# Kernel tuning notes

Measured on AMD Instinct MI355X. Metric: run time of the kernel, lower is better.

Reference implementation:

```python
import jax, jax.numpy as jnp
import numpy as np

EPS = 1e-5

def l2norm(x, axis=-1):
    # matches torch F.normalize(p=2): denom clamped at 1e-12
    n = jnp.linalg.norm(x, axis=axis, keepdims=True)
    return x / jnp.maximum(n, 1e-12)

def setup_inputs() -> dict:
    key = jax.random.key(0)
    ks = jax.random.split(key, 10)
    B, N, D, P = 8, 1024, 128, 16
    context = jax.random.normal(ks[0], (B, N, D), jnp.float32)
    acc_u = jax.random.normal(ks[1], (B, N, 1), jnp.float32)
    acc_v = jax.random.normal(ks[2], (B, N, 1), jnp.float32)
    uv_angle = jax.random.normal(ks[3], (B, N, 1), jnp.float32)
    uv_angleACC = jax.random.normal(ks[4], (B, N, 1), jnp.float32)
    speed = jax.random.normal(ks[5], (B, N, 1), jnp.float32)
    dist = jax.random.uniform(ks[6], (N, N), jnp.float32)
    angle = jax.random.normal(ks[7], (N, N), jnp.float32)
    # xavier_uniform for weight_tensor [P, D]: bound = sqrt(6/(P+D))
    bound = float(np.sqrt(6.0 / (P + D)))
    weight_tensor = jax.random.uniform(ks[8], (P, D), jnp.float32, -bound, bound)
    return {"context": context, "acc_u": acc_u, "acc_v": acc_v,
            "uv_angle": uv_angle, "uv_angleACC": uv_angleACC, "speed": speed,
            "isPhy": 1, "dist": dist, "angle": angle,
            "weight_tensor": weight_tensor}

def reference(context, acc_u, acc_v, uv_angle, uv_angleACC, speed, isPhy, dist, angle, weight_tensor):
    gamma, theta, sigma = 1.4, 0.5, 0.5
    P = weight_tensor.shape[0]
    N = context.shape[1]
    # --- weighted-cosine multi-perspective attention ---
    w = weight_tensor[:, None, None, :]                 # [P,1,1,D]
    context_fc = context[None] * w                      # [P,B,N,D]
    context_norm = l2norm(context_fc)                   # [P,B,N,D]
    # matmul over perspectives then mean over P
    attention = jnp.einsum('pbnd,pbmd->bnm', context_norm, context_norm) / P
    # --- epsilon neighbourhood (epsilon=0, markoff=0), mask detached ---
    mask = jax.lax.stop_gradient((attention > 0.0).astype(attention.dtype))
    attention = attention * mask
    # --- wind dynamics (pred_var 'u', isPhy True, dist given) ---
    Acc = acc_u * acc_u + acc_v * acc_v                 # [B,N,1]
    x1 = jnp.sqrt(Acc[:, :, 0] + EPS)                   # [B,N]
    x2 = jnp.abs(jnp.cos(uv_angleACC[:, :, 0] - uv_angle[:, :, 0]))
    temp_acc = x1 * x2                                  # [B,N]
    acc_part = temp_acc[:, :, None] * jnp.eye(N, dtype=attention.dtype)  # diag [B,N,N]
    spd = jax.lax.stop_gradient(speed)                  # speed.detach()
    ang = jax.lax.stop_gradient(angle)[None]            # torch.tensor() detaches
    d = jax.lax.stop_gradient(dist)[None] + EPS
    # uv_angle/speed broadcast [B,N,1] -> [B,N,N] (repeat along last dim)
    selfwind = jnp.abs(spd) * jnp.abs(jnp.cos(ang - uv_angle) + sigma * acc_part) / d
    selfwind = l2norm(selfwind)                         # [B,N,N]
    y = gamma * jnp.einsum('bnk,bmk->bnm', selfwind, selfwind) / 20.0 + EPS
    y = l2norm(y)
    u = l2norm(jnp.abs(theta * selfwind + jnp.sqrt(y)) + EPS)
    return attention * u
```

## Files before the change

kernel.cpp:

```cpp
#include <hip/hip_runtime.h>
#include <hip/hip_bf16.h>
#include <math.h>

#define EPSV 1e-5f
#define AS1 __attribute__((address_space(1)))
#define AS3 __attribute__((address_space(3)))

typedef __attribute__((ext_vector_type(4))) float f32x4;
typedef __attribute__((ext_vector_type(8))) short bf16x8;
typedef __attribute__((ext_vector_type(4))) unsigned short u16x4;

__device__ __forceinline__ unsigned short f2b(float x) {
  union { float f; unsigned int u; } v; v.f = x;
  unsigned int r = v.u + 0x7FFFu + ((v.u >> 16) & 1u);
  return (unsigned short)(r >> 16);
}
__device__ __forceinline__ float b2f(unsigned short h) {
  union { float f; unsigned int u; } v; v.u = ((unsigned int)h) << 16;
  return v.f;
}

__device__ __forceinline__ float block_reduce_sum(float v, float* sbuf) {
  #pragma unroll
  for (int off = 32; off; off >>= 1) v += __shfl_xor(v, off);
  __syncthreads();
  if ((threadIdx.x & 63) == 0) sbuf[threadIdx.x >> 6] = v;
  __syncthreads();
  return sbuf[0] + sbuf[1] + sbuf[2] + sbuf[3];
}

__global__ __launch_bounds__(256) void prep(const float* __restrict__ ctx,
                                            const float* __restrict__ wt,
                                            const float* __restrict__ speed,
                                            const float* __restrict__ uva,
                                            const float* __restrict__ accu,
                                            const float* __restrict__ accv,
                                            const float* __restrict__ uvaACC,
                                            const float* __restrict__ angle,
                                            const float* __restrict__ dist,
                                            unsigned short* __restrict__ V,
                                            unsigned short* __restrict__ SW,
                                            int N) {
  __shared__ float sbuf[4];
  const int bn = blockIdx.x;
  const int tid = threadIdx.x;

  {
    const int w = tid >> 6;
    const int lane = tid & 63;
    const int p = w * 4 + (lane >> 4);
    const int dl = (lane & 15) * 8;
    const float* c = ctx + (size_t)bn * 128;
    const f32x4 ca = *(const f32x4*)(c + dl);
    const f32x4 cb = *(const f32x4*)(c + dl + 4);
    const f32x4 wa = *(const f32x4*)(wt + p * 128 + dl);
    const f32x4 wb = *(const f32x4*)(wt + p * 128 + dl + 4);
    float a[8];
    float ss = 0.0f;
    #pragma unroll
    for (int i = 0; i < 4; ++i) {
      a[i] = ca[i] * wa[i];
      a[4 + i] = cb[i] * wb[i];
      ss += a[i] * a[i] + a[4 + i] * a[4 + i];
    }
    ss += __shfl_xor(ss, 1);
    ss += __shfl_xor(ss, 2);
    ss += __shfl_xor(ss, 4);
    ss += __shfl_xor(ss, 8);
    const float inv = 1.0f / fmaxf(sqrtf(ss), 1e-12f);
    bf16x8 o;
    #pragma unroll
    for (int i = 0; i < 8; ++i) o[i] = (short)f2b(a[i] * inv);
    *(bf16x8*)(V + (size_t)bn * 2048 + p * 128 + dl) = o;
  }

  {
    const int n = bn & (N - 1);
    const float ua = uva[bn];
    const float sp = fabsf(speed[bn]);
    const float au = accu[bn], av = accv[bn];
    const float ta = sqrtf(au * au + av * av + EPSV) * fabsf(cosf(uvaACC[bn] - ua));
    const f32x4 an = *(const f32x4*)(angle + (size_t)n * N + 4 * tid);
    const f32x4 dv = *(const f32x4*)(dist + (size_t)n * N + 4 * tid);
    float v[4];
    float ss = 0.0f;
    #pragma unroll
    for (int i = 0; i < 4; ++i) {
      float cv = cosf(an[i] - ua);
      if (4 * tid + i == n) cv += 0.5f * ta;
      v[i] = sp * fabsf(cv) / (dv[i] + EPSV);
      ss += v[i] * v[i];
    }
    ss = block_reduce_sum(ss, sbuf);
    const float inv = 1.0f / fmaxf(sqrtf(ss), 1e-12f);
    u16x4 o;
    #pragma unroll
    for (int i = 0; i < 4; ++i) o[i] = f2b(v[i] * inv);
    *(u16x4*)(SW + (size_t)bn * N + 4 * tid) = o;
  }
}

#define FENCE asm volatile("" ::: "memory")
__device__ __forceinline__ void barx() { FENCE; __builtin_amdgcn_s_barrier(); FENCE; }

template <bool ATTB>
__global__ __launch_bounds__(512, 4) void gemm8(const unsigned short* __restrict__ V,
                                                const unsigned short* __restrict__ SW,
                                                float* __restrict__ OUT,
                                                unsigned short* __restrict__ Yb,
                                                unsigned short* __restrict__ ATT,
                                                int boff) {
  __shared__ __align__(16) unsigned short As[3][128 * 32];
  __shared__ __align__(16) unsigned short Bs[3][256 * 32];
  const int id = blockIdx.x + boff;
  const bool att = id < 256;
  const int r = att ? id : id - 256;
  const int b = r & 7;
  const int tile = r >> 3;
  const int m0 = (tile & 7) * 128;
  const int n0 = (tile >> 3) * 256;
  const int K = att ? 2048 : 1024;
  const int NN = 1024;
  const unsigned short* Ab = att ? (V + (size_t)b * NN * 2048) : (SW + (size_t)b * NN * NN);

  const int tid = threadIdx.x;
  const int lane = tid & 63;
  const int wid = tid >> 6;
  const int wm = (wid >> 2) * 64;
  const int wn = (wid & 3) * 64;
  const int fr = lane & 15;
  const int fc = lane >> 4;
  const int rsw = (fc ^ ((fr >> 1) & 3)) << 3;

  f32x4 acc[4][4] = {};
  bf16x8 af[4], bf[4];

  auto stage = [&](int sb, int kt) {
    const int k0 = kt << 5;
    {
      const int row = tid >> 2;
      const int c = (tid & 3) ^ ((row >> 1) & 3);
      __builtin_amdgcn_global_load_lds(
          (const AS1 unsigned int*)(Ab + (size_t)(m0 + row) * K + k0 + (c << 3)),
          (AS3 unsigned int*)(&As[sb][tid * 8]), 16, 0, 0);
    }
    #pragma unroll
    for (int e = 0; e < 2; ++e) {
      const int idx = e * 512 + tid;
      const int row = idx >> 2;
      const int c = (idx & 3) ^ ((row >> 1) & 3);
      __builtin_amdgcn_global_load_lds(
          (const AS1 unsigned int*)(Ab + (size_t)(n0 + row) * K + k0 + (c << 3)),
          (AS3 unsigned int*)(&Bs[sb][idx * 8]), 16, 0, 0);
    }
  };

  const int nk = K >> 5;

  stage(0, 0);
  stage(1, 1);
  asm volatile("s_waitcnt vmcnt(3)" ::: "memory");
  barx();

  int rd = 0;
  for (int t = 0; t < nk; ++t) {
    if (t + 2 < nk) {
      int st = rd + 2; if (st >= 3) st -= 3;
      stage(st, t + 2);
    }
    const unsigned short* Ar = As[rd];
    const unsigned short* Br = Bs[rd];
    #pragma unroll
    for (int i = 0; i < 4; ++i)
      af[i] = *(const bf16x8*)(Ar + (wm + i * 16 + fr) * 32 + rsw);
    #pragma unroll
    for (int j = 0; j < 4; ++j)
      bf[j] = *(const bf16x8*)(Br + (wn + j * 16 + fr) * 32 + rsw);
    __builtin_amdgcn_s_setprio(1);
    #pragma unroll
    for (int i = 0; i < 4; ++i)
      #pragma unroll
      for (int j = 0; j < 4; ++j)
        acc[i][j] = __builtin_amdgcn_mfma_f32_16x16x32_bf16(af[i], bf[j], acc[i][j], 0, 0, 0);
    __builtin_amdgcn_s_setprio(0);
    if (t + 2 < nk)      { asm volatile("s_waitcnt vmcnt(3)" ::: "memory"); }
    else if (t + 1 < nk) { asm volatile("s_waitcnt vmcnt(0)" ::: "memory"); }
    barx();
    rd = (rd + 1 == 3) ? 0 : rd + 1;
  }

  if (att) {
    if (ATTB) {
      unsigned short* Cb = ATT + (size_t)b * NN * NN;
      #pragma unroll
      for (int i = 0; i < 4; ++i)
        #pragma unroll
        for (int rr = 0; rr < 4; ++rr) {
          const int row = m0 + wm + i * 16 + fc * 4 + rr;
          #pragma unroll
          for (int j = 0; j < 4; ++j) {
            const int col = n0 + wn + j * 16 + fr;
            Cb[(size_t)row * NN + col] = f2b(fmaxf(acc[i][j][rr] * (1.0f / 16.0f), 0.0f));
          }
        }
    } else {
      float* Cb = OUT + (size_t)b * NN * NN;
      #pragma unroll
      for (int i = 0; i < 4; ++i)
        #pragma unroll
        for (int rr = 0; rr < 4; ++rr) {
          const int row = m0 + wm + i * 16 + fc * 4 + rr;
          #pragma unroll
          for (int j = 0; j < 4; ++j) {
            const int col = n0 + wn + j * 16 + fr;
            Cb[(size_t)row * NN + col] = fmaxf(acc[i][j][rr] * (1.0f / 16.0f), 0.0f);
          }
        }
    }
  } else {
    unsigned short* Cb = Yb + (size_t)b * NN * NN;
    #pragma unroll
    for (int i = 0; i < 4; ++i)
      #pragma unroll
      for (int rr = 0; rr < 4; ++rr) {
        const int row = m0 + wm + i * 16 + fc * 4 + rr;
        #pragma unroll
        for (int j = 0; j < 4; ++j) {
          const int col = n0 + wn + j * 16 + fr;
          Cb[(size_t)row * NN + col] = f2b(acc[i][j][rr] * (1.4f / 20.0f) + EPSV);
        }
      }
  }
}

template <bool ATTB>
__global__ __launch_bounds__(256) void finkern(const unsigned short* __restrict__ Yb,
                                               const unsigned short* __restrict__ SW,
                                               const unsigned short* __restrict__ ATT,
                                               float* __restrict__ OUT) {
  const int row = blockIdx.x * 4 + (threadIdx.x >> 6);
  const int lane = threadIdx.x & 63;
  const unsigned short* y = Yb + (size_t)row * 1024;
  const unsigned short* sw = SW + (size_t)row * 1024;
  float* o = OUT + (size_t)row * 1024;

  float yv[16];
  float ss = 0.0f;
  #pragma unroll
  for (int ch = 0; ch < 4; ++ch) {
    const u16x4 yr = *(const u16x4*)(y + ch * 256 + lane * 4);
    #pragma unroll
    for (int i = 0; i < 4; ++i) {
      yv[ch * 4 + i] = b2f(yr[i]);
      ss += yv[ch * 4 + i] * yv[ch * 4 + i];
    }
  }
  #pragma unroll
  for (int off = 32; off; off >>= 1) ss += __shfl_xor(ss, off);
  const float invy = 1.0f / fmaxf(sqrtf(ss), 1e-12f);

  float tv[16];
  float st = 0.0f;
  #pragma unroll
  for (int ch = 0; ch < 4; ++ch) {
    const u16x4 sr = *(const u16x4*)(sw + ch * 256 + lane * 4);
    #pragma unroll
    for (int i = 0; i < 4; ++i) {
      const float x = fabsf(0.5f * b2f(sr[i]) + sqrtf(yv[ch * 4 + i] * invy)) + EPSV;
      tv[ch * 4 + i] = x;
      st += x * x;
    }
  }
  #pragma unroll
  for (int off = 32; off; off >>= 1) st += __shfl_xor(st, off);
  const float invt = 1.0f / fmaxf(sqrtf(st), 1e-12f);

  if (ATTB) {
    const unsigned short* at = ATT + (size_t)row * 1024;
    #pragma unroll
    for (int ch = 0; ch < 4; ++ch) {
      const u16x4 ar = *(const u16x4*)(at + ch * 256 + lane * 4);
      f32x4 ov;
      #pragma unroll
      for (int i = 0; i < 4; ++i) ov[i] = b2f(ar[i]) * (tv[ch * 4 + i] * invt);
      *(f32x4*)(o + ch * 256 + lane * 4) = ov;
    }
  } else {
    #pragma unroll
    for (int ch = 0; ch < 4; ++ch) {
      f32x4 ov = *(f32x4*)(o + ch * 256 + lane * 4);
      #pragma unroll
      for (int i = 0; i < 4; ++i) ov[i] *= tv[ch * 4 + i] * invt;
      *(f32x4*)(o + ch * 256 + lane * 4) = ov;
    }
  }
}

extern "C" void kernel_launch(void* const* d_in, const int* in_sizes, int n_in,
                              void* d_out, int out_size, void* d_ws, size_t ws_size,
                              hipStream_t stream) {
  const float* ctx        = (const float*)d_in[0];
  const float* acc_u      = (const float*)d_in[1];
  const float* acc_v      = (const float*)d_in[2];
  const float* uv_angle   = (const float*)d_in[3];
  const float* uv_angleACC= (const float*)d_in[4];
  const float* speed      = (const float*)d_in[5];
  const float* dist       = (const float*)d_in[7];
  const float* angle      = (const float*)d_in[8];
  const float* wt         = (const float*)d_in[9];

  const int B = 8, N = 1024, P = 16;
  const int K1 = P * 128;
  const int BN = B * N;

  const size_t szV  = (size_t)BN * K1 * 2;
  const size_t szSW = (size_t)BN * N * 2;
  const size_t szYb = (size_t)BN * N * 2;
  const size_t szA  = (size_t)BN * N * 2;

  unsigned short* V  = (unsigned short*)d_ws;
  unsigned short* SW = (unsigned short*)((char*)d_ws + szV);
  float* out = (float*)d_out;

  prep<<<dim3(BN), dim3(256), 0, stream>>>(ctx, wt, speed, uv_angle, acc_u,
                                           acc_v, uv_angleACC, angle, dist,
                                           V, SW, N);

  if (ws_size >= szV + szSW + szYb + szA) {
    unsigned short* Yp = (unsigned short*)((char*)d_ws + szV + szSW);
    unsigned short* At = (unsigned short*)((char*)d_ws + szV + szSW + szYb);
    gemm8<true><<<dim3(512), dim3(512), 0, stream>>>(V, SW, out, Yp, At, 0);
    finkern<true><<<dim3(BN / 4), dim3(256), 0, stream>>>(Yp, SW, At, out);
  } else if (ws_size >= szV + szSW + szYb) {
    unsigned short* Yp = (unsigned short*)((char*)d_ws + szV + szSW);
    gemm8<false><<<dim3(512), dim3(512), 0, stream>>>(V, SW, out, Yp, nullptr, 0);
    finkern<false><<<dim3(BN / 4), dim3(256), 0, stream>>>(Yp, SW, nullptr, out);
  } else {
    unsigned short* Yp = (unsigned short*)d_ws;
    gemm8<false><<<dim3(256), dim3(512), 0, stream>>>(V, SW, out, Yp, nullptr, 0);
    gemm8<false><<<dim3(256), dim3(512), 0, stream>>>(V, SW, out, Yp, nullptr, 256);
    finkern<false><<<dim3(BN / 4), dim3(256), 0, stream>>>(Yp, SW, nullptr, out);
  }
}
```

Measured before the change: 169.7 us.

## Exploit Gram-matrix symmetry: compute upper-triangle tiles only and mirror stores

Both batched GEMMs produce symmetric Gram matrices (V·Vᵀ and SW·SWᵀ), so the kernel now computes only the 36 upper-triangular 128x128 tiles per batch and writes each off-diagonal tile twice, once transposed. This roughly halves the MFMA work and operand loads. Tiles shrink from 128x256 with 512 threads to 128x128 with 256 threads, attention and Y tiles are interleaved in one launch, and the prefetch issue point and barrier placement in the K loop move. The cost is extra strided transposed stores and a different occupancy and tiling balance.

```diff
diff --git a/kernel.cpp b/kernel.cpp
--- a/kernel.cpp
+++ b/kernel.cpp
@@ -104,30 +104,34 @@
 __device__ __forceinline__ void barx() { FENCE; __builtin_amdgcn_s_barrier(); FENCE; }
 
 template <bool ATTB>
-__global__ __launch_bounds__(512, 4) void gemm8(const unsigned short* __restrict__ V,
+__global__ __launch_bounds__(256, 3) void gemmT(const unsigned short* __restrict__ V,
                                                 const unsigned short* __restrict__ SW,
                                                 float* __restrict__ OUT,
                                                 unsigned short* __restrict__ Yb,
                                                 unsigned short* __restrict__ ATT,
-                                                int boff) {
+                                                int mode) {
   __shared__ __align__(16) unsigned short As[3][128 * 32];
-  __shared__ __align__(16) unsigned short Bs[3][256 * 32];
-  const int id = blockIdx.x + boff;
-  const bool att = id < 256;
-  const int r = att ? id : id - 256;
+  __shared__ __align__(16) unsigned short Bs[3][128 * 32];
+  const int id = blockIdx.x;
+  const bool isatt = (mode == 0) ? ((id & 1) == 0) : (mode == 1);
+  const int r = (mode == 0) ? (id >> 1) : id;
   const int b = r & 7;
-  const int tile = r >> 3;
-  const int m0 = (tile & 7) * 128;
-  const int n0 = (tile >> 3) * 256;
-  const int K = att ? 2048 : 1024;
+  int t = r >> 3;
+  int ti = 0;
+  while (t >= 8 - ti) { t -= 8 - ti; ++ti; }
+  const int tj = ti + t;
+  const int m0 = ti * 128;
+  const int n0 = tj * 128;
+  const int K = isatt ? 2048 : 1024;
   const int NN = 1024;
-  const unsigned short* Ab = att ? (V + (size_t)b * NN * 2048) : (SW + (size_t)b * NN * NN);
+  const unsigned short* Ab = isatt ? (V + (size_t)b * NN * 2048)
+                                   : (SW + (size_t)b * NN * NN);
 
   const int tid = threadIdx.x;
   const int lane = tid & 63;
   const int wid = tid >> 6;
-  const int wm = (wid >> 2) * 64;
-  const int wn = (wid & 3) * 64;
+  const int wm = (wid >> 1) * 64;
+  const int wn = (wid & 1) * 64;
   const int fr = lane & 15;
   const int fc = lane >> 4;
   const int rsw = (fc ^ ((fr >> 1) & 3)) << 3;
@@ -137,19 +141,15 @@
 
   auto stage = [&](int sb, int kt) {
     const int k0 = kt << 5;
-    {
-      const int row = tid >> 2;
-      const int c = (tid & 3) ^ ((row >> 1) & 3);
-      __builtin_amdgcn_global_load_lds(
-          (const AS1 unsigned int*)(Ab + (size_t)(m0 + row) * K + k0 + (c << 3)),
-          (AS3 unsigned int*)(&As[sb][tid * 8]), 16, 0, 0);
-    }
     #pragma unroll
     for (int e = 0; e < 2; ++e) {
-      const int idx = e * 512 + tid;
+      const int idx = e * 256 + tid;
       const int row = idx >> 2;
       const int c = (idx & 3) ^ ((row >> 1) & 3);
       __builtin_amdgcn_global_load_lds(
+          (const AS1 unsigned int*)(Ab + (size_t)(m0 + row) * K + k0 + (c << 3)),
+          (AS3 unsigned int*)(&As[sb][idx * 8]), 16, 0, 0);
+      __builtin_amdgcn_global_load_lds(
           (const AS1 unsigned int*)(Ab + (size_t)(n0 + row) * K + k0 + (c << 3)),
           (AS3 unsigned int*)(&Bs[sb][idx * 8]), 16, 0, 0);
     }
@@ -159,15 +159,11 @@
 
   stage(0, 0);
   stage(1, 1);
-  asm volatile("s_waitcnt vmcnt(3)" ::: "memory");
+  asm volatile("s_waitcnt vmcnt(4)" ::: "memory");
   barx();
 
   int rd = 0;
-  for (int t = 0; t < nk; ++t) {
-    if (t + 2 < nk) {
-      int st = rd + 2; if (st >= 3) st -= 3;
-      stage(st, t + 2);
-    }
+  for (int kt = 0; kt < nk; ++kt) {
     const unsigned short* Ar = As[rd];
     const unsigned short* Br = Bs[rd];
     #pragma unroll
@@ -176,6 +172,13 @@
     #pragma unroll
     for (int j = 0; j < 4; ++j)
       bf[j] = *(const bf16x8*)(Br + (wn + j * 16 + fr) * 32 + rsw);
+
+    if (kt + 2 < nk) {
+      int st = rd + 2; if (st >= 3) st -= 3;
+      stage(st, kt + 2);
+    }
+    barx();
+    asm volatile("s_waitcnt lgkmcnt(0)" ::: "memory");
     __builtin_amdgcn_s_setprio(1);
     #pragma unroll
     for (int i = 0; i < 4; ++i)
@@ -183,52 +186,49 @@
       for (int j = 0; j < 4; ++j)
         acc[i][j] = __builtin_amdgcn_mfma_f32_16x16x32_bf16(af[i], bf[j], acc[i][j], 0, 0, 0);
     __builtin_amdgcn_s_setprio(0);
-    if (t + 2 < nk)      { asm volatile("s_waitcnt vmcnt(3)" ::: "memory"); }
-    else if (t + 1 < nk) { asm volatile("s_waitcnt vmcnt(0)" ::: "memory"); }
+    if (kt + 2 < nk)      { asm volatile("s_waitcnt vmcnt(4)" ::: "memory"); }
+    else if (kt + 1 < nk) { asm volatile("s_waitcnt vmcnt(0)" ::: "memory"); }
     barx();
     rd = (rd + 1 == 3) ? 0 : rd + 1;
   }
 
-  if (att) {
-    if (ATTB) {
-      unsigned short* Cb = ATT + (size_t)b * NN * NN;
-      #pragma unroll
-      for (int i = 0; i < 4; ++i)
+  const bool mirror = (ti != tj);
+  if (isatt && !ATTB) {
+    float* Cb = OUT + (size_t)b * NN * NN;
+    #pragma unroll
+    for (int i = 0; i < 4; ++i)
+      #pragma unroll
+      for (int j = 0; j < 4; ++j) {
+        const int col = n0 + wn + j * 16 + fr;
+        const int rowb = m0 + wm + i * 16 + fc * 4;
+        f32x4 tv;
         #pragma unroll
         for (int rr = 0; rr < 4; ++rr) {
-          const int row = m0 + wm + i * 16 + fc * 4 + rr;
-          #pragma unroll
-          for (int j = 0; j < 4; ++j) {
-            const int col = n0 + wn + j * 16 + fr;
-            Cb[(size_t)row * NN + col] = f2b(fmaxf(acc[i][j][rr] * (1.0f / 16.0f), 0.0f));
-          }
+          const float v = fmaxf(acc[i][j][rr] * (1.0f / 16.0f), 0.0f);
+          Cb[(size_t)(rowb + rr) * NN + col] = v;
+          tv[rr] = v;
         }
-    } else {
-      float* Cb = OUT + (size_t)b * NN * NN;
-      #pragma unroll
-      for (int i = 0; i < 4; ++i)
+        if (mirror) *(f32x4*)(Cb + (size_t)col * NN + rowb) = tv;
+      }
+  } else {
+    unsigned short* Cb = (isatt ? ATT : Yb) + (size_t)b * NN * NN;
+    const float scale = isatt ? (1.0f / 16.0f) : (1.4f / 20.0f);
+    #pragma unroll
+    for (int i = 0; i < 4; ++i)
+      #pragma unroll
+      for (int j = 0; j < 4; ++j) {
+        const int col = n0 + wn + j * 16 + fr;
+        const int rowb = m0 + wm + i * 16 + fc * 4;
+        u16x4 tv;
         #pragma unroll
         for (int rr = 0; rr < 4; ++rr) {
-          const int row = m0 + wm + i * 16 + fc * 4 + rr;
-          #pragma unroll
-          for (int j = 0; j < 4; ++j) {
-            const int col = n0 + wn + j * 16 + fr;
-            Cb[(size_t)row * NN + col] = fmaxf(acc[i][j][rr] * (1.0f / 16.0f), 0.0f);
-          }
+          const float v = isatt ? fmaxf(acc[i][j][rr] * scale, 0.0f)
+                                : (acc[i][j][rr] * scale + EPSV);
+          const unsigned short h = f2b(v);
+          Cb[(size_t)(rowb + rr) * NN + col] = h;
+          tv[rr] = h;
         }
-    }
-  } else {
-    unsigned short* Cb = Yb + (size_t)b * NN * NN;
-    #pragma unroll
-    for (int i = 0; i < 4; ++i)
-      #pragma unroll
-      for (int rr = 0; rr < 4; ++rr) {
-        const int row = m0 + wm + i * 16 + fc * 4 + rr;
-        #pragma unroll
-        for (int j = 0; j < 4; ++j) {
-          const int col = n0 + wn + j * 16 + fr;
-          Cb[(size_t)row * NN + col] = f2b(acc[i][j][rr] * (1.4f / 20.0f) + EPSV);
-        }
+        if (mirror) *(u16x4*)(Cb + (size_t)col * NN + rowb) = tv;
       }
   }
 }
@@ -329,16 +329,16 @@
   if (ws_size >= szV + szSW + szYb + szA) {
     unsigned short* Yp = (unsigned short*)((char*)d_ws + szV + szSW);
     unsigned short* At = (unsigned short*)((char*)d_ws + szV + szSW + szYb);
-    gemm8<true><<<dim3(512), dim3(512), 0, stream>>>(V, SW, out, Yp, At, 0);
+    gemmT<true><<<dim3(576), dim3(256), 0, stream>>>(V, SW, out, Yp, At, 0);
     finkern<true><<<dim3(BN / 4), dim3(256), 0, stream>>>(Yp, SW, At, out);
   } else if (ws_size >= szV + szSW + szYb) {
     unsigned short* Yp = (unsigned short*)((char*)d_ws + szV + szSW);
-    gemm8<false><<<dim3(512), dim3(512), 0, stream>>>(V, SW, out, Yp, nullptr, 0);
+    gemmT<false><<<dim3(576), dim3(256), 0, stream>>>(V, SW, out, Yp, nullptr, 0);
     finkern<false><<<dim3(BN / 4), dim3(256), 0, stream>>>(Yp, SW, nullptr, out);
   } else {
     unsigned short* Yp = (unsigned short*)d_ws;
-    gemm8<false><<<dim3(256), dim3(512), 0, stream>>>(V, SW, out, Yp, nullptr, 0);
-    gemm8<false><<<dim3(256), dim3(512), 0, stream>>>(V, SW, out, Yp, nullptr, 256);
+    gemmT<false><<<dim3(288), dim3(256), 0, stream>>>(V, SW, out, Yp, nullptr, 1);
+    gemmT<false><<<dim3(288), dim3(256), 0, stream>>>(V, SW, out, Yp, nullptr, 2);
     finkern<false><<<dim3(BN / 4), dim3(256), 0, stream>>>(Yp, SW, nullptr, out);
   }
 }
```

Result: no change. 167.9 us (-1.0%).
